# Kernel tuning notes

Hardware: AMD Instinct MI355X
Metric: run time of the kernel (lower is better)

The kernel has to match this reference:

```python
import jax, jax.numpy as jnp
import numpy as np
from jax import lax

DIM = 512          # input channels
H_IN = 56          # input spatial size
B = 32             # batch
C = DIM // 4       # inner attention dim = 128
WS = H_IN // 4     # window size = 14
NH = 4             # num_heads (C > 64 branch)
HD = C // NH       # head dim = 32
N = WS * WS        # tokens = 196
BN_EPS = 1e-5


def _rel_index():
    # Swin-style relative position index, matches the torch buffer computation.
    coords = np.stack(np.meshgrid(np.arange(WS), np.arange(WS), indexing='ij'))  # [2,WS,WS]
    flat = coords.reshape(2, -1)                                                 # [2,N]
    rel = (flat[:, :, None] - flat[:, None, :]).transpose(1, 2, 0).astype(np.int64)  # [N,N,2]
    rel[..., 0] += WS - 1
    rel[..., 1] += WS - 1
    rel[..., 0] *= 2 * WS - 1
    return jnp.asarray(rel.sum(-1))  # [N,N] int


def _interp_mat(n_in, scale):
    # Bilinear upsample (align_corners=True, as in nn.UpsamplingBilinear2d) as a matrix.
    n_out = n_in * scale
    src = np.arange(n_out) * (n_in - 1) / (n_out - 1)
    lo = np.floor(src).astype(np.int64)
    hi = np.minimum(lo + 1, n_in - 1)
    w = (src - lo).astype(np.float32)
    M = np.zeros((n_out, n_in), np.float32)
    M[np.arange(n_out), lo] += 1.0 - w
    M[np.arange(n_out), hi] += w
    return jnp.asarray(M)  # [n_out, n_in]


def setup_inputs() -> dict:
    key = jax.random.key(0)
    ks = jax.random.split(key, 8)
    x = jax.random.normal(ks[0], (B, DIM, H_IN, H_IN), jnp.float32)
    # grouped 4x4/stride-4 conv: groups = C, in_per_group = DIM // C = 4 -> OIHW [C,4,4,4]
    conv_w = jax.random.normal(ks[1], (C, 4, 4, 4), jnp.float32) * 0.05
    conv_b = jnp.zeros((C,), jnp.float32)
    bn_gamma = jnp.ones((C,), jnp.float32)
    bn_beta = jnp.zeros((C,), jnp.float32)
    bn_mean = jnp.zeros((C,), jnp.float32)
    bn_var = jnp.ones((C,), jnp.float32)
    qkv_w = jax.random.normal(ks[2], (3 * C, C), jnp.float32) * (C ** -0.5)
    proj_w = jax.random.normal(ks[3], (C, C), jnp.float32) * (C ** -0.5)
    proj_b = jnp.zeros((C,), jnp.float32)
    rpb_table = jax.random.normal(ks[4], ((2 * WS - 1) ** 2, NH), jnp.float32) * 0.02
    convout_w = jax.random.normal(ks[5], (DIM, C), jnp.float32) * (C ** -0.5)
    convout_b = jnp.zeros((DIM,), jnp.float32)
    return dict(x=x, conv_w=conv_w, conv_b=conv_b, bn_gamma=bn_gamma, bn_beta=bn_beta,
                bn_mean=bn_mean, bn_var=bn_var, qkv_w=qkv_w, proj_w=proj_w, proj_b=proj_b,
                rpb_table=rpb_table, convout_w=convout_w, convout_b=convout_b)


def reference(x, conv_w, conv_b, bn_gamma, bn_beta, bn_mean, bn_var,
              qkv_w, proj_w, proj_b, rpb_table, convout_w, convout_b):
    # local_embed: grouped conv 4x4 s4 -> BN (eval) -> ReLU6
    y = lax.conv_general_dilated(x, conv_w, window_strides=(4, 4), padding='VALID',
                                 dimension_numbers=('NCHW', 'OIHW', 'NCHW'),
                                 feature_group_count=C)
    y = y + conv_b[None, :, None, None]
    scale_bn = bn_gamma * lax.rsqrt(bn_var + BN_EPS)
    y = y * scale_bn[None, :, None, None] + (bn_beta - bn_mean * scale_bn)[None, :, None, None]
    y = jnp.clip(y, 0.0, 6.0)  # ReLU6

    # flatten to tokens: [B, N, C]
    t = y.reshape(B, C, N).transpose(0, 2, 1)

    # qkv projection (no bias) -> q,k,v [B, NH, N, HD]
    qkv = (t @ qkv_w.T).reshape(B, N, 3, NH, HD).transpose(2, 0, 3, 1, 4)
    q, k, v = qkv[0], qkv[1], qkv[2]
    q = q * (HD ** -0.5)

    attn = jnp.einsum('bhnd,bhmd->bhnm', q, k)  # [B,NH,N,N]
    idx = _rel_index()                           # [N,N]
    bias = rpb_table[idx.reshape(-1)].reshape(N, N, NH).transpose(2, 0, 1)  # [NH,N,N]
    attn = jax.nn.softmax(attn + bias[None], axis=-1)

    o = jnp.einsum('bhnm,bhmd->bhnd', attn, v)  # [B,NH,N,HD]
    o = o.transpose(0, 2, 1, 3).reshape(B, N, C)
    o = o @ proj_w.T + proj_b

    # blc2bchw
    o = o.reshape(B, WS, WS, C).transpose(0, 3, 1, 2)  # [B,C,WS,WS]

    # 1x1 conv back to DIM channels
    o = jnp.einsum('oc,bchw->bohw', convout_w, o) + convout_b[None, :, None, None]

    # bilinear upsample x4, align_corners=True
    M = _interp_mat(WS, 4)  # [4*WS, WS]
    o = jnp.einsum('Oh,bchw->bcOw', M, o)
    o = jnp.einsum('Pw,bchw->bchP', M, o)
    return o  # [B, DIM, H_IN, H_IN]
```

## Files before the change

### kernel.cpp

```cpp
#include <hip/hip_runtime.h>

#define QSCALE 0.17677669529663687f

__global__ __launch_bounds__(256) void conv_embed_kernel(
    const float* __restrict__ x, const float* __restrict__ cw,
    const float* __restrict__ cb, const float* __restrict__ gam,
    const float* __restrict__ bet, const float* __restrict__ mea,
    const float* __restrict__ var, float* __restrict__ tbuf)
{
  __shared__ __align__(16) float xs[12544];
  __shared__ __align__(16) float wsm[64];
  const int c = blockIdx.x, b = blockIdx.y, tid = threadIdx.x;
  const float4* xb = (const float4*)(x + (b*512 + 4*c)*3136);
  for (int t = tid; t < 3136; t += 256) ((float4*)xs)[t] = xb[t];
  if (tid < 64) wsm[tid] = cw[c*64 + tid];
  __syncthreads();
  if (tid < 196) {
    int oy = tid / 14, ox = tid - (tid/14)*14;
    float acc = cb[c];
#pragma unroll
    for (int i = 0; i < 4; ++i)
#pragma unroll
      for (int kh = 0; kh < 4; ++kh) {
        float4 xv = *(const float4*)&xs[i*3136 + (4*oy+kh)*56 + 4*ox];
        float4 wv = *(const float4*)&wsm[i*16 + kh*4];
        acc += xv.x*wv.x + xv.y*wv.y + xv.z*wv.z + xv.w*wv.w;
      }
    float sc = gam[c] * rsqrtf(var[c] + 1e-5f);
    float v = acc*sc + (bet[c] - mea[c]*sc);
    v = fminf(fmaxf(v, 0.0f), 6.0f);
    tbuf[(b*196 + tid)*128 + c] = v;
  }
}

__global__ __launch_bounds__(256) void make_wc_kernel(
    const float* __restrict__ cow, const float* __restrict__ pw,
    const float* __restrict__ pb, const float* __restrict__ cob,
    float* __restrict__ Wc, float* __restrict__ bias_c)
{
  int idx = blockIdx.x*256 + threadIdx.x;
  int oc = idx >> 7, k = idx & 127;
  float acc = 0.f;
  for (int cc = 0; cc < 128; ++cc) acc += cow[oc*128 + cc] * pw[cc*128 + k];
  Wc[idx] = acc;
  if (blockIdx.x < 2) {
    float a2 = cob[idx];
    for (int cc = 0; cc < 128; ++cc) a2 += cow[idx*128 + cc] * pb[cc];
    bias_c[idx] = a2;
  }
}

__device__ __forceinline__ void gemm_tile_64x64(
    const float* __restrict__ Ag, const float* __restrict__ Bg,
    int row0, int col0, float* As, float* Bs, float (&acc)[4][4])
{
  const int tid = threadIdx.x;
#pragma unroll
  for (int it = 0; it < 8; ++it) {
    int rr = (it & 3)*16 + (tid & 15);
    int kq = (it >> 2)*16 + (tid >> 4);
    float4 va = *(const float4*)&Ag[(row0+rr)*128 + kq*4];
    As[(4*kq+0)*68 + rr] = va.x;
    As[(4*kq+1)*68 + rr] = va.y;
    As[(4*kq+2)*68 + rr] = va.z;
    As[(4*kq+3)*68 + rr] = va.w;
    float4 vb = *(const float4*)&Bg[(col0+rr)*128 + kq*4];
    Bs[(4*kq+0)*68 + rr] = vb.x;
    Bs[(4*kq+1)*68 + rr] = vb.y;
    Bs[(4*kq+2)*68 + rr] = vb.z;
    Bs[(4*kq+3)*68 + rr] = vb.w;
  }
  __syncthreads();
  const int tx = (tid & 15)*4, ty = (tid >> 4)*4;
#pragma unroll 8
  for (int k = 0; k < 128; ++k) {
    float4 a4 = *(const float4*)&As[k*68 + ty];
    float4 b4 = *(const float4*)&Bs[k*68 + tx];
    float av[4] = {a4.x, a4.y, a4.z, a4.w};
    float bv[4] = {b4.x, b4.y, b4.z, b4.w};
#pragma unroll
    for (int i = 0; i < 4; ++i)
#pragma unroll
      for (int j = 0; j < 4; ++j) acc[i][j] += av[i]*bv[j];
  }
}

__global__ __launch_bounds__(256) void gemm_qkv_kernel(
    const float* __restrict__ t, const float* __restrict__ qkv_w,
    float* __restrict__ qkv)
{
  __shared__ __align__(16) float As[128*68];
  __shared__ __align__(16) float Bs[128*68];
  float acc[4][4] = {};
  gemm_tile_64x64(t, qkv_w, blockIdx.y*64, blockIdx.x*64, As, Bs, acc);
  const int tid = threadIdx.x;
  const int tx = (tid & 15)*4, ty = (tid >> 4)*4;
#pragma unroll
  for (int i = 0; i < 4; ++i) {
    int row = blockIdx.y*64 + ty + i;
    int bb = row / 196, nn = row - bb*196;
#pragma unroll
    for (int j = 0; j < 4; ++j) {
      int col = blockIdx.x*64 + tx + j;
      int s3 = col >> 7, rr = col & 127;
      int hh = rr >> 5, dd = rr & 31;
      float v = acc[i][j];
      if (s3 == 0) v *= QSCALE;
      qkv[(((s3*32 + bb)*4 + hh)*196 + nn)*32 + dd] = v;
    }
  }
}

__global__ __launch_bounds__(256) void attn_kernel(
    const float* __restrict__ qkv, const float* __restrict__ rpb,
    float* __restrict__ o)
{
  __shared__ __align__(16) float k_lds[256*36];
  __shared__ __align__(16) float v_lds[196*36];
  __shared__ __align__(16) float q_lds[100*32];
  __shared__ float rpb_lds[732];
  __shared__ float p_lds[16*200];
  const int half = blockIdx.x, h = blockIdx.y, b = blockIdx.z;
  const int tid = threadIdx.x;
  const int n0 = half*98;
  const float* qg = qkv + ((0*32 + b)*4 + h)*6272 + n0*32;
  const float* kg = qkv + ((1*32 + b)*4 + h)*6272;
  const float* vg = qkv + ((2*32 + b)*4 + h)*6272;
  for (int t4 = tid; t4 < 1568; t4 += 256) {
    float4 kv = ((const float4*)kg)[t4];
    float4 vv = ((const float4*)vg)[t4];
    int m = t4 >> 3, d = (t4 & 7)*4;
    float* kp = &k_lds[m*36 + d];
    kp[0]=kv.x; kp[1]=kv.y; kp[2]=kv.z; kp[3]=kv.w;
    float* vp = &v_lds[m*36 + d];
    vp[0]=vv.x; vp[1]=vv.y; vp[2]=vv.z; vp[3]=vv.w;
  }
  for (int t4 = tid; t4 < 784; t4 += 256)
    ((float4*)q_lds)[t4] = ((const float4*)qg)[t4];
  for (int t = tid; t < 729; t += 256) rpb_lds[t] = rpb[t*4 + h];
  __syncthreads();
  const int l = tid & 63, w = tid >> 6;
  const int mg = l >> 3, d4 = l & 7;
  for (int g = w; g < 25; g += 4) {
    const int rcnt = (g == 24) ? 2 : 4;
    float s[4][4];
#pragma unroll
    for (int r = 0; r < 4; ++r)
#pragma unroll
      for (int it = 0; it < 4; ++it) s[r][it] = 0.f;
#pragma unroll
    for (int d8 = 0; d8 < 8; ++d8) {
      float4 q4[4];
#pragma unroll
      for (int r = 0; r < 4; ++r)
        q4[r] = *(const float4*)&q_lds[(g*4+r)*32 + d8*4];
#pragma unroll
      for (int it = 0; it < 4; ++it) {
        int m = it*64 + l;
        float4 k4 = *(const float4*)&k_lds[m*36 + d8*4];
#pragma unroll
        for (int r = 0; r < 4; ++r)
          s[r][it] += q4[r].x*k4.x + q4[r].y*k4.y + q4[r].z*k4.z + q4[r].w*k4.w;
      }
    }
    float mx[4] = {-1e30f, -1e30f, -1e30f, -1e30f};
    int yn[4], xn[4];
#pragma unroll
    for (int r = 0; r < 4; ++r) {
      int n = n0 + g*4 + r; if (n > 195) n = 195;
      yn[r] = n / 14; xn[r] = n - yn[r]*14;
    }
#pragma unroll
    for (int it = 0; it < 4; ++it) {
      int m = it*64 + l;
      if (m < 196) {
        int ym = m / 14, xm = m - ym*14;
#pragma unroll
        for (int r = 0; r < 4; ++r) {
          s[r][it] += rpb_lds[(yn[r]-ym+13)*27 + (xn[r]-xm+13)];
          mx[r] = fmaxf(mx[r], s[r][it]);
        }
      }
    }
#pragma unroll
    for (int off = 32; off > 0; off >>= 1)
#pragma unroll
      for (int r = 0; r < 4; ++r)
        mx[r] = fmaxf(mx[r], __shfl_xor(mx[r], off));
    float sum[4] = {0.f, 0.f, 0.f, 0.f};
#pragma unroll
    for (int it = 0; it < 4; ++it) {
      int m = it*64 + l;
      if (m < 196) {
#pragma unroll
        for (int r = 0; r < 4; ++r) {
          float p = __expf(s[r][it] - mx[r]);
          sum[r] += p;
          p_lds[(w*4+r)*200 + m] = p;
        }
      }
    }
#pragma unroll
    for (int off = 32; off > 0; off >>= 1)
#pragma unroll
      for (int r = 0; r < 4; ++r)
        sum[r] += __shfl_xor(sum[r], off);
    float4 acc[4];
#pragma unroll
    for (int r = 0; r < 4; ++r) acc[r] = make_float4(0.f, 0.f, 0.f, 0.f);
    for (int t = 0; t < 25; ++t) {
      int m = t*8 + mg;
      if (m < 196) {
        float4 v4 = *(const float4*)&v_lds[m*36 + d4*4];
#pragma unroll
        for (int r = 0; r < 4; ++r) {
          float p = p_lds[(w*4+r)*200 + m];
          acc[r].x += p*v4.x; acc[r].y += p*v4.y;
          acc[r].z += p*v4.z; acc[r].w += p*v4.w;
        }
      }
    }
#pragma unroll
    for (int off = 8; off < 64; off <<= 1)
#pragma unroll
      for (int r = 0; r < 4; ++r) {
        acc[r].x += __shfl_xor(acc[r].x, off);
        acc[r].y += __shfl_xor(acc[r].y, off);
        acc[r].z += __shfl_xor(acc[r].z, off);
        acc[r].w += __shfl_xor(acc[r].w, off);
      }
    if (mg == 0) {
      for (int r = 0; r < rcnt; ++r) {
        int n = n0 + g*4 + r;
        float iv = 1.f / sum[r];
        float4 ov = make_float4(acc[r].x*iv, acc[r].y*iv, acc[r].z*iv, acc[r].w*iv);
        *((float4*)&o[(b*196 + n)*128 + h*32 + d4*4]) = ov;
      }
    }
  }
}

__global__ __launch_bounds__(256) void gemm_out_kernel(
    const float* __restrict__ obuf, const float* __restrict__ Wc,
    const float* __restrict__ bias_c, float* __restrict__ co)
{
  __shared__ __align__(16) float As[128*68];
  __shared__ __align__(16) float Bs[128*68];
  float acc[4][4] = {};
  gemm_tile_64x64(obuf, Wc, blockIdx.y*64, blockIdx.x*64, As, Bs, acc);
  const int tid = threadIdx.x;
  const int tx = (tid & 15)*4, ty = (tid >> 4)*4;
#pragma unroll
  for (int i = 0; i < 4; ++i) {
    int row = blockIdx.y*64 + ty + i;
    int bb = row / 196, nn = row - bb*196;
#pragma unroll
    for (int j = 0; j < 4; ++j) {
      int col = blockIdx.x*64 + tx + j;
      co[(bb*512 + col)*196 + nn] = acc[i][j] + bias_c[col];
    }
  }
}

__global__ __launch_bounds__(256) void upsample_kernel(
    const float* __restrict__ co, float* __restrict__ out)
{
  __shared__ float cs[1568];
  __shared__ int lo_s[56];
  __shared__ float w_s[56];
  const int cg = blockIdx.x, b = blockIdx.y, tid = threadIdx.x;
  const float* cbase = co + (b*512 + cg*8)*196;
  for (int t = tid; t < 1568; t += 256) cs[t] = cbase[t];
  if (tid < 56) {
    double s = (double)(tid*13) / 55.0;
    int lo = (int)s;
    lo_s[tid] = lo;
    w_s[tid] = (float)(s - lo);
  }
  __syncthreads();
  float* obase = out + (b*512 + cg*8)*3136;
  for (int t4 = tid; t4 < 6272; t4 += 256) {
    int ch = t4 / 784;
    int rem = t4 - ch*784;
    int i2 = rem / 14;
    int j4 = (rem - i2*14)*4;
    int li = lo_s[i2]; float wi = w_s[i2];
    int hi = (li+1 < 13) ? li+1 : 13;
    const float* p0 = cs + ch*196 + li*14;
    const float* p1 = cs + ch*196 + hi*14;
    float4 ov;
    float* ovp = (float*)&ov;
#pragma unroll
    for (int jj = 0; jj < 4; ++jj) {
      int j2 = j4 + jj;
      int lj = lo_s[j2]; float wj = w_s[j2];
      int hj = (lj+1 < 13) ? lj+1 : 13;
      float top = p0[lj]*(1.f-wj) + p0[hj]*wj;
      float bot = p1[lj]*(1.f-wj) + p1[hj]*wj;
      ovp[jj] = top*(1.f-wi) + bot*wi;
    }
    ((float4*)obase)[t4] = ov;
  }
}

extern "C" void kernel_launch(void* const* d_in, const int* in_sizes, int n_in,
                              void* d_out, int out_size, void* d_ws, size_t ws_size,
                              hipStream_t stream)
{
  const float* x         = (const float*)d_in[0];
  const float* conv_w    = (const float*)d_in[1];
  const float* conv_b    = (const float*)d_in[2];
  const float* bn_gamma  = (const float*)d_in[3];
  const float* bn_beta   = (const float*)d_in[4];
  const float* bn_mean   = (const float*)d_in[5];
  const float* bn_var    = (const float*)d_in[6];
  const float* qkv_w     = (const float*)d_in[7];
  const float* proj_w    = (const float*)d_in[8];
  const float* proj_b    = (const float*)d_in[9];
  const float* rpb       = (const float*)d_in[10];
  const float* convout_w = (const float*)d_in[11];
  const float* convout_b = (const float*)d_in[12];
  float* out = (float*)d_out;
  float* ws  = (float*)d_ws;

  float* tbuf   = ws;
  float* qkvb   = ws + 802816;
  float* obuf   = ws + 3211264;
  float* Wc     = ws + 4014080;
  float* bias_c = ws + 4079616;
  float* co     = ws + 4080128;

  conv_embed_kernel<<<dim3(128, 32), 256, 0, stream>>>(
      x, conv_w, conv_b, bn_gamma, bn_beta, bn_mean, bn_var, tbuf);
  make_wc_kernel<<<dim3(256), 256, 0, stream>>>(
      convout_w, proj_w, proj_b, convout_b, Wc, bias_c);
  gemm_qkv_kernel<<<dim3(6, 98), 256, 0, stream>>>(tbuf, qkv_w, qkvb);
  attn_kernel<<<dim3(2, 4, 32), 256, 0, stream>>>(qkvb, rpb, obuf);
  gemm_out_kernel<<<dim3(8, 98), 256, 0, stream>>>(obuf, Wc, bias_c, co);
  upsample_kernel<<<dim3(64, 32), 256, 0, stream>>>(co, out);
}
```

Measured before the change: 517.8 us.

## Split attention into tiled score GEMM and softmax-PV kernels; vectorize epilogue stores

The fused attention kernel is replaced by two kernels. The first computes Q·K^T plus the relative position bias as a 64x64 register-tiled GEMM over 16 tiles per head and writes the scores to a global scratch buffer. The second reads those scores, does the softmax and multiplies by V, with one thread per query row. The QKV and output GEMM epilogues now write float4 vectors instead of scalar stores. This is meant to raise parallelism and compute efficiency in attention, at the cost of an extra global round trip for the score matrix and a poorly occupied softmax kernel (49 of 64 threads active). The score scratch buffer also aliases the output-conv buffer, which only works if it is no longer needed by then and the workspace is large enough.

```diff
diff --git a/kernel.cpp b/kernel.cpp
--- a/kernel.cpp
+++ b/kernel.cpp
@@ -95,147 +95,137 @@
   gemm_tile_64x64(t, qkv_w, blockIdx.y*64, blockIdx.x*64, As, Bs, acc);
   const int tid = threadIdx.x;
   const int tx = (tid & 15)*4, ty = (tid >> 4)*4;
+  const int col0 = blockIdx.x*64 + tx;
+  const int s3 = col0 >> 7, rr = col0 & 127;
+  const int hh = rr >> 5, dd = rr & 31;
+  const float qs = (s3 == 0) ? QSCALE : 1.0f;
 #pragma unroll
   for (int i = 0; i < 4; ++i) {
     int row = blockIdx.y*64 + ty + i;
     int bb = row / 196, nn = row - bb*196;
-#pragma unroll
-    for (int j = 0; j < 4; ++j) {
-      int col = blockIdx.x*64 + tx + j;
-      int s3 = col >> 7, rr = col & 127;
-      int hh = rr >> 5, dd = rr & 31;
-      float v = acc[i][j];
-      if (s3 == 0) v *= QSCALE;
-      qkv[(((s3*32 + bb)*4 + hh)*196 + nn)*32 + dd] = v;
+    float4 v;
+    v.x = acc[i][0]*qs; v.y = acc[i][1]*qs; v.z = acc[i][2]*qs; v.w = acc[i][3]*qs;
+    *(float4*)&qkv[(((s3*32 + bb)*4 + hh)*196 + nn)*32 + dd] = v;
+  }
+}
+
+__global__ __launch_bounds__(256) void score_kernel(
+    const float* __restrict__ qkv, const float* __restrict__ rpb,
+    float* __restrict__ St)
+{
+  __shared__ __align__(16) float Ks[32*68];
+  __shared__ __align__(16) float Qs[32*68];
+  __shared__ float rpb_lds[729];
+  const int tile = blockIdx.x, h = blockIdx.y, b = blockIdx.z;
+  const int tm = (tile >> 2)*64, tn = (tile & 3)*64;
+  const int tid = threadIdx.x;
+  const float* qg = qkv + (b*4 + h)*6272;
+  const float* kg = qkv + ((32 + b)*4 + h)*6272;
+#pragma unroll
+  for (int it = 0; it < 2; ++it) {
+    int rr = (tid & 31) + it*32;
+    int kq = tid >> 5;
+    int rk = tm + rr; if (rk > 195) rk = 195;
+    float4 va = *(const float4*)&kg[rk*32 + kq*4];
+    Ks[(4*kq+0)*68+rr] = va.x; Ks[(4*kq+1)*68+rr] = va.y;
+    Ks[(4*kq+2)*68+rr] = va.z; Ks[(4*kq+3)*68+rr] = va.w;
+    int rq = tn + rr; if (rq > 195) rq = 195;
+    float4 vb = *(const float4*)&qg[rq*32 + kq*4];
+    Qs[(4*kq+0)*68+rr] = vb.x; Qs[(4*kq+1)*68+rr] = vb.y;
+    Qs[(4*kq+2)*68+rr] = vb.z; Qs[(4*kq+3)*68+rr] = vb.w;
+  }
+  for (int t = tid; t < 729; t += 256) rpb_lds[t] = rpb[t*4 + h];
+  __syncthreads();
+  const int tx = (tid & 15)*4, ty = (tid >> 4)*4;
+  float acc[4][4] = {};
+#pragma unroll 8
+  for (int k = 0; k < 32; ++k) {
+    float4 a4 = *(const float4*)&Ks[k*68 + ty];
+    float4 b4 = *(const float4*)&Qs[k*68 + tx];
+    float av[4] = {a4.x, a4.y, a4.z, a4.w};
+    float bv[4] = {b4.x, b4.y, b4.z, b4.w};
+#pragma unroll
+    for (int i = 0; i < 4; ++i)
+#pragma unroll
+      for (int j = 0; j < 4; ++j) acc[i][j] += av[i]*bv[j];
+  }
+  int ym[4], xm[4], yn[4], xn[4];
+#pragma unroll
+  for (int i = 0; i < 4; ++i) {
+    int m = tm + ty + i; if (m > 195) m = 0;
+    ym[i] = m / 14; xm[i] = m - ym[i]*14;
+  }
+#pragma unroll
+  for (int j = 0; j < 4; ++j) {
+    int n = tn + tx + j; if (n > 195) n = 0;
+    yn[j] = n / 14; xn[j] = n - yn[j]*14;
+  }
+  float* stb = St + ((b*4 + h)*196)*200;
+  const bool nfull = (tn + tx + 3 < 196);
+#pragma unroll
+  for (int i = 0; i < 4; ++i) {
+    int m = tm + ty + i;
+    if (m >= 196) continue;
+    float sv[4];
+#pragma unroll
+    for (int j = 0; j < 4; ++j)
+      sv[j] = acc[i][j] + rpb_lds[(yn[j]-ym[i]+13)*27 + (xn[j]-xm[i]+13)];
+    if (nfull) {
+      float4 v4; v4.x = sv[0]; v4.y = sv[1]; v4.z = sv[2]; v4.w = sv[3];
+      *(float4*)&stb[m*200 + tn + tx] = v4;
+    } else {
+#pragma unroll
+      for (int j = 0; j < 4; ++j)
+        if (tn + tx + j < 196) stb[m*200 + tn + tx + j] = sv[j];
     }
   }
 }
 
-__global__ __launch_bounds__(256) void attn_kernel(
-    const float* __restrict__ qkv, const float* __restrict__ rpb,
+__global__ __launch_bounds__(64) void softmax_pv_kernel(
+    const float* __restrict__ qkv, const float* __restrict__ St,
     float* __restrict__ o)
 {
-  __shared__ __align__(16) float k_lds[256*36];
-  __shared__ __align__(16) float v_lds[196*36];
-  __shared__ __align__(16) float q_lds[100*32];
-  __shared__ float rpb_lds[732];
-  __shared__ float p_lds[16*200];
-  const int half = blockIdx.x, h = blockIdx.y, b = blockIdx.z;
-  const int tid = threadIdx.x;
-  const int n0 = half*98;
-  const float* qg = qkv + ((0*32 + b)*4 + h)*6272 + n0*32;
-  const float* kg = qkv + ((1*32 + b)*4 + h)*6272;
-  const float* vg = qkv + ((2*32 + b)*4 + h)*6272;
-  for (int t4 = tid; t4 < 1568; t4 += 256) {
-    float4 kv = ((const float4*)kg)[t4];
-    float4 vv = ((const float4*)vg)[t4];
-    int m = t4 >> 3, d = (t4 & 7)*4;
-    float* kp = &k_lds[m*36 + d];
-    kp[0]=kv.x; kp[1]=kv.y; kp[2]=kv.z; kp[3]=kv.w;
-    float* vp = &v_lds[m*36 + d];
-    vp[0]=vv.x; vp[1]=vv.y; vp[2]=vv.z; vp[3]=vv.w;
-  }
-  for (int t4 = tid; t4 < 784; t4 += 256)
-    ((float4*)q_lds)[t4] = ((const float4*)qg)[t4];
-  for (int t = tid; t < 729; t += 256) rpb_lds[t] = rpb[t*4 + h];
-  __syncthreads();
-  const int l = tid & 63, w = tid >> 6;
-  const int mg = l >> 3, d4 = l & 7;
-  for (int g = w; g < 25; g += 4) {
-    const int rcnt = (g == 24) ? 2 : 4;
-    float s[4][4];
-#pragma unroll
-    for (int r = 0; r < 4; ++r)
-#pragma unroll
-      for (int it = 0; it < 4; ++it) s[r][it] = 0.f;
-#pragma unroll
-    for (int d8 = 0; d8 < 8; ++d8) {
-      float4 q4[4];
-#pragma unroll
-      for (int r = 0; r < 4; ++r)
-        q4[r] = *(const float4*)&q_lds[(g*4+r)*32 + d8*4];
-#pragma unroll
-      for (int it = 0; it < 4; ++it) {
-        int m = it*64 + l;
-        float4 k4 = *(const float4*)&k_lds[m*36 + d8*4];
-#pragma unroll
-        for (int r = 0; r < 4; ++r)
-          s[r][it] += q4[r].x*k4.x + q4[r].y*k4.y + q4[r].z*k4.z + q4[r].w*k4.w;
-      }
+  __shared__ __align__(16) float v_lds[196*32];
+  const int q4 = blockIdx.x, h = blockIdx.y, b = blockIdx.z;
+  const int tid = threadIdx.x;
+  const float4* vg = (const float4*)(qkv + ((64 + b)*4 + h)*6272);
+  for (int t = tid; t < 1568; t += 64) ((float4*)v_lds)[t] = vg[t];
+  __syncthreads();
+  const int row = q4*49 + tid;
+  const bool act = (tid < 49);
+  const int rowc = act ? row : q4*49;
+  const float* sp = St + ((b*4 + h)*196)*200 + rowc;
+  float mx = -1e30f;
+  for (int m = 0; m < 196; m += 4) {
+    float s0 = sp[(m+0)*200], s1 = sp[(m+1)*200];
+    float s2 = sp[(m+2)*200], s3 = sp[(m+3)*200];
+    mx = fmaxf(mx, fmaxf(fmaxf(s0, s1), fmaxf(s2, s3)));
+  }
+  float4 oa[8];
+#pragma unroll
+  for (int d = 0; d < 8; ++d) oa[d] = make_float4(0.f, 0.f, 0.f, 0.f);
+  float sum = 0.f;
+#pragma unroll 2
+  for (int m = 0; m < 196; ++m) {
+    float e = __expf(sp[m*200] - mx);
+    sum += e;
+    const float4* vr = (const float4*)&v_lds[m*32];
+#pragma unroll
+    for (int d = 0; d < 8; ++d) {
+      float4 v4 = vr[d];
+      oa[d].x += e*v4.x; oa[d].y += e*v4.y;
+      oa[d].z += e*v4.z; oa[d].w += e*v4.w;
     }
-    float mx[4] = {-1e30f, -1e30f, -1e30f, -1e30f};
-    int yn[4], xn[4];
-#pragma unroll
-    for (int r = 0; r < 4; ++r) {
-      int n = n0 + g*4 + r; if (n > 195) n = 195;
-      yn[r] = n / 14; xn[r] = n - yn[r]*14;
-    }
-#pragma unroll
-    for (int it = 0; it < 4; ++it) {
-      int m = it*64 + l;
-      if (m < 196) {
-        int ym = m / 14, xm = m - ym*14;
-#pragma unroll
-        for (int r = 0; r < 4; ++r) {
-          s[r][it] += rpb_lds[(yn[r]-ym+13)*27 + (xn[r]-xm+13)];
-          mx[r] = fmaxf(mx[r], s[r][it]);
-        }
-      }
-    }
-#pragma unroll
-    for (int off = 32; off > 0; off >>= 1)
-#pragma unroll
-      for (int r = 0; r < 4; ++r)
-        mx[r] = fmaxf(mx[r], __shfl_xor(mx[r], off));
-    float sum[4] = {0.f, 0.f, 0.f, 0.f};
-#pragma unroll
-    for (int it = 0; it < 4; ++it) {
-      int m = it*64 + l;
-      if (m < 196) {
-#pragma unroll
-        for (int r = 0; r < 4; ++r) {
-          float p = __expf(s[r][it] - mx[r]);
-          sum[r] += p;
-          p_lds[(w*4+r)*200 + m] = p;
-        }
-      }
-    }
-#pragma unroll
-    for (int off = 32; off > 0; off >>= 1)
-#pragma unroll
-      for (int r = 0; r < 4; ++r)
-        sum[r] += __shfl_xor(sum[r], off);
-    float4 acc[4];
-#pragma unroll
-    for (int r = 0; r < 4; ++r) acc[r] = make_float4(0.f, 0.f, 0.f, 0.f);
-    for (int t = 0; t < 25; ++t) {
-      int m = t*8 + mg;
-      if (m < 196) {
-        float4 v4 = *(const float4*)&v_lds[m*36 + d4*4];
-#pragma unroll
-        for (int r = 0; r < 4; ++r) {
-          float p = p_lds[(w*4+r)*200 + m];
-          acc[r].x += p*v4.x; acc[r].y += p*v4.y;
-          acc[r].z += p*v4.z; acc[r].w += p*v4.w;
-        }
-      }
-    }
-#pragma unroll
-    for (int off = 8; off < 64; off <<= 1)
-#pragma unroll
-      for (int r = 0; r < 4; ++r) {
-        acc[r].x += __shfl_xor(acc[r].x, off);
-        acc[r].y += __shfl_xor(acc[r].y, off);
-        acc[r].z += __shfl_xor(acc[r].z, off);
-        acc[r].w += __shfl_xor(acc[r].w, off);
-      }
-    if (mg == 0) {
-      for (int r = 0; r < rcnt; ++r) {
-        int n = n0 + g*4 + r;
-        float iv = 1.f / sum[r];
-        float4 ov = make_float4(acc[r].x*iv, acc[r].y*iv, acc[r].z*iv, acc[r].w*iv);
-        *((float4*)&o[(b*196 + n)*128 + h*32 + d4*4]) = ov;
-      }
+  }
+  if (act) {
+    float inv = 1.f / sum;
+    float4* op = (float4*)&o[(b*196 + row)*128 + h*32];
+#pragma unroll
+    for (int d = 0; d < 8; ++d) {
+      float4 v4;
+      v4.x = oa[d].x*inv; v4.y = oa[d].y*inv;
+      v4.z = oa[d].z*inv; v4.w = oa[d].w*inv;
+      op[d] = v4;
     }
   }
 }
@@ -250,15 +240,16 @@
   gemm_tile_64x64(obuf, Wc, blockIdx.y*64, blockIdx.x*64, As, Bs, acc);
   const int tid = threadIdx.x;
   const int tx = (tid & 15)*4, ty = (tid >> 4)*4;
-#pragma unroll
-  for (int i = 0; i < 4; ++i) {
-    int row = blockIdx.y*64 + ty + i;
-    int bb = row / 196, nn = row - bb*196;
-#pragma unroll
-    for (int j = 0; j < 4; ++j) {
-      int col = blockIdx.x*64 + tx + j;
-      co[(bb*512 + col)*196 + nn] = acc[i][j] + bias_c[col];
-    }
+  const int row0 = blockIdx.y*64 + ty;
+  const int bb = row0 / 196, nn0 = row0 - bb*196;
+#pragma unroll
+  for (int j = 0; j < 4; ++j) {
+    int col = blockIdx.x*64 + tx + j;
+    float bc = bias_c[col];
+    float4 v;
+    v.x = acc[0][j] + bc; v.y = acc[1][j] + bc;
+    v.z = acc[2][j] + bc; v.w = acc[3][j] + bc;
+    *(float4*)&co[(bb*512 + col)*196 + nn0] = v;
   }
 }
 
@@ -328,6 +319,7 @@
   float* obuf   = ws + 3211264;
   float* Wc     = ws + 4014080;
   float* bias_c = ws + 4079616;
+  float* St     = ws + 4080128;
   float* co     = ws + 4080128;
 
   conv_embed_kernel<<<dim3(128, 32), 256, 0, stream>>>(
@@ -335,7 +327,8 @@
   make_wc_kernel<<<dim3(256), 256, 0, stream>>>(
       convout_w, proj_w, proj_b, convout_b, Wc, bias_c);
   gemm_qkv_kernel<<<dim3(6, 98), 256, 0, stream>>>(tbuf, qkv_w, qkvb);
-  attn_kernel<<<dim3(2, 4, 32), 256, 0, stream>>>(qkvb, rpb, obuf);
+  score_kernel<<<dim3(16, 4, 32), 256, 0, stream>>>(qkvb, rpb, St);
+  softmax_pv_kernel<<<dim3(4, 4, 32), 64, 0, stream>>>(qkvb, St, obuf);
   gemm_out_kernel<<<dim3(8, 98), 256, 0, stream>>>(obuf, Wc, bias_c, co);
   upsample_kernel<<<dim3(64, 32), 256, 0, stream>>>(co, out);
 }
```

After: 503.2 us. -2.8%, faster.
